# Kernel optimization log

Hardware: AMD Instinct MI355X
Metric: run time of the kernel (lower is better)

The kernel has to match this reference:

```python
import jax, jax.numpy as jnp
import numpy as np

B, N, HID = 2, 512, 768
BIAF = 256
CLS = 14
CH = 32
SIZE_DIM = 25
N_POS = 30
HSZ = 2 * (BIAF + 1) + SIZE_DIM


def setup_inputs() -> dict:
    key = jax.random.key(0)
    ks = jax.random.split(key, 16)
    s = 0.02
    return {
        "x": jax.random.normal(ks[0], (B, N, HID), jnp.float32),
        "y": jax.random.normal(ks[1], (B, N, HID), jnp.float32),
        "z": jax.random.normal(ks[2], (B, N, N, CH), jnp.float32),
        "mlp1_w": jax.random.normal(ks[3], (BIAF, HID), jnp.float32) * s,
        "mlp1_b": jnp.zeros((BIAF,), jnp.float32),
        "mlp2_w": jax.random.normal(ks[4], (BIAF, HID), jnp.float32) * s,
        "mlp2_b": jnp.zeros((BIAF,), jnp.float32),
        "head_w": jax.random.normal(ks[5], (BIAF, HID), jnp.float32) * s,
        "head_b": jnp.zeros((BIAF,), jnp.float32),
        "tail_w": jax.random.normal(ks[6], (BIAF, HID), jnp.float32) * s,
        "tail_b": jnp.zeros((BIAF,), jnp.float32),
        "biaf_W": jax.random.normal(ks[7], (CLS, BIAF + 1, BIAF + 1), jnp.float32) * s,
        "W": jax.random.normal(ks[8], (CLS, HSZ), jnp.float32) * s,
        "size_emb": jax.random.normal(ks[9], (N_POS, SIZE_DIM), jnp.float32) * s,
    }


def reference(x, y, z, mlp1_w, mlp1_b, mlp2_w, mlp2_b, head_w, head_b,
              tail_w, tail_b, biaf_W, W, size_emb):
    # MLP branches (dropout=0 at eval; torch GELU is exact erf)
    h = jax.nn.gelu(x @ mlp1_w.T + mlp1_b, approximate=False)   # (b,m,BIAF)
    t = jax.nn.gelu(y @ mlp2_w.T + mlp2_b, approximate=False)   # (b,n,BIAF)
    ones = jnp.ones(h.shape[:-1] + (1,), h.dtype)
    h1 = jnp.concatenate([h, ones], -1)                          # (b,m,BIAF+1)
    t1 = jnp.concatenate([t, ones], -1)                          # (b,n,BIAF+1)
    # Biaffine with bias_x=bias_y=True -> (b,cls,m,n)
    o1 = jnp.einsum('bmi,kij,bnj->bkmn', h1, biaf_W, t1)

    # head/tail MLPs with LeakyReLU(0.01), then append 1-column
    head = jax.nn.leaky_relu(x @ head_w.T + head_b, 0.01)
    tail = jax.nn.leaky_relu(x @ tail_w.T + tail_b, 0.01)
    head = jnp.concatenate([head, ones], -1)                     # (b,m,BIAF+1)
    tail = jnp.concatenate([tail, ones], -1)                     # (b,n,BIAF+1)

    # einsum('bmnh,kh->bkmn', cat([head_m, tail_n, size_mn]), W) decomposed so
    # the (b,m,n,HSZ) pairwise tensor is never materialized (same math).
    d = head.shape[-1]
    Wh, Wt, Ws = W[:, :d], W[:, d:2 * d], W[:, 2 * d:]
    n = x.shape[1]
    ar = jnp.arange(n)
    ids = jnp.clip(ar[None, :] - ar[:, None], -N_POS // 2, N_POS // 2 - 1) + N_POS // 2
    se = size_emb[ids]                                           # (m,n,SIZE_DIM)
    o3 = (jnp.einsum('bmh,kh->bkm', head, Wh)[:, :, :, None]
          + jnp.einsum('bnh,kh->bkn', tail, Wt)[:, :, None, :]
          + jnp.einsum('mnh,kh->kmn', se, Ws)[None])
    return o1 + o3
```

## Files before the change

### kernel.cpp

```cpp
#include <hip/hip_runtime.h>
#include <hip/hip_bf16.h>
#include <math.h>

#define BDIM 2
#define NDIM 512
#define HID 768
#define BIAF 256
#define CLS 14
#define DD 257
#define NPOS 30
#define SDIM 25
#define HSZ 539
#define PK 288
#define PJ 384
#define LDW 40

typedef unsigned short ushort_t;
typedef __attribute__((ext_vector_type(8))) short short8;
typedef __attribute__((ext_vector_type(4))) float floatx4;

#define MFMA16(a, b, c) __builtin_amdgcn_mfma_f32_16x16x32_bf16((a), (b), (c), 0, 0, 0)

__device__ inline float bf2f(ushort_t u) {
    union { unsigned int i; float f; } c; c.i = ((unsigned)u) << 16; return c.f;
}
__device__ inline ushort_t f2bf(float f) {
    __hip_bfloat16 h = __float2bfloat16(f);
    return *(ushort_t*)&h;
}

__device__ inline void split8(const float* v, short8& hi, short8& lo) {
    #pragma unroll
    for (int j = 0; j < 8; ++j) {
        ushort_t h = f2bf(v[j]);
        float hf = bf2f(h);
        ((short*)&hi)[j] = (short)h;
        ((short*)&lo)[j] = (short)f2bf(v[j] - hf);
    }
}

__device__ inline void stage_tile(const ushort_t* __restrict__ g, size_t gstride,
                                  ushort_t* __restrict__ lds, int tid) {
    int r0 = tid >> 2, c4 = tid & 3;
    #pragma unroll
    for (int i = 0; i < 2; ++i) {
        int row = i * 64 + r0;
        uint4 v = *(const uint4*)(g + (size_t)row * gstride + c4 * 8);
        *(uint4*)(lds + row * LDW + c4 * 8) = v;
    }
}

__global__ __launch_bounds__(256) void repack_t(
    const float* __restrict__ biafW, ushort_t* __restrict__ packW)
{
    __shared__ float tile[32][33];
    const int i0 = blockIdx.x * 32;
    const int j0 = blockIdx.y * 32;
    const int k  = blockIdx.z;
    const int r8 = threadIdx.x >> 5;
    const int c  = threadIdx.x & 31;
    #pragma unroll
    for (int rr = 0; rr < 4; ++rr) {
        int r = rr * 8 + r8;
        int gi = i0 + r, gj = j0 + c;
        tile[r][c] = (gi < DD && gj < DD) ? biafW[((size_t)k * DD + gi) * DD + gj] : 0.f;
    }
    __syncthreads();
    #pragma unroll
    for (int rr = 0; rr < 4; ++rr) {
        int jr = rr * 8 + r8;
        packW[((size_t)k * PJ + (j0 + jr)) * PK + i0 + c] = f2bf(tile[c][jr]);
    }
}

__global__ __launch_bounds__(256) void wsplit(
    const float* __restrict__ m1w, const float* __restrict__ m2w,
    const float* __restrict__ hw,  const float* __restrict__ tw,
    ushort_t* __restrict__ whi, ushort_t* __restrict__ wlo)
{
    int idx = blockIdx.x * 256 + threadIdx.x;
    int mat = idx / (BIAF * HID);
    int rem = idx % (BIAF * HID);
    const float* src = (mat == 0) ? m1w : (mat == 1) ? m2w : (mat == 2) ? hw : tw;
    float v = src[rem];
    ushort_t h = f2bf(v);
    whi[idx] = h;
    wlo[idx] = f2bf(v - bf2f(h));
}

__global__ void fill_pads(ushort_t* __restrict__ h1hi, ushort_t* __restrict__ h1lo,
                          ushort_t* __restrict__ t1hi, ushort_t* __restrict__ t1lo) {
    int idx = blockIdx.x * 256 + threadIdx.x;
    int plane = idx >> 15;
    int tok = (idx >> 5) & 1023;
    int c   = 256 + (idx & 31);
    ushort_t* dst = (plane == 0) ? h1hi : (plane == 1) ? h1lo : (plane == 2) ? t1hi : t1lo;
    ushort_t val = (c == 256 && (plane == 0 || plane == 2)) ? (ushort_t)0x3F80 : (ushort_t)0;
    dst[(size_t)tok * PK + c] = val;
}

__global__ __launch_bounds__(256) void proj_mfma(
    const float* __restrict__ x, const float* __restrict__ y,
    const ushort_t* __restrict__ whi, const ushort_t* __restrict__ wlo,
    const float* __restrict__ m1b, const float* __restrict__ m2b,
    const float* __restrict__ hb,  const float* __restrict__ tb,
    ushort_t* __restrict__ h1hi, ushort_t* __restrict__ h1lo,
    ushort_t* __restrict__ t1hi, ushort_t* __restrict__ t1lo,
    float* __restrict__ headf, float* __restrict__ tailf)
{
    const int bx = blockIdx.x;
    const int proj = bx >> 6;
    const int mt = (bx >> 2) & 15;
    const int ft = bx & 3;
    const int wave = threadIdx.x >> 6, L = threadIdx.x & 63;
    const int quad = L >> 4, l16 = L & 15;
    const int m0w = mt * 64 + wave * 16;
    const int f0 = ft * 64;

    const float* src  = (proj == 1) ? y : x;
    const float* bias = (proj == 0) ? m1b : (proj == 1) ? m2b : (proj == 2) ? hb : tb;

    const float* arow = src + (size_t)(m0w + l16) * HID + quad * 8;
    const size_t wbase = (size_t)proj * BIAF * HID;

    floatx4 acc[4];
    #pragma unroll
    for (int nf = 0; nf < 4; ++nf)
        #pragma unroll
        for (int r = 0; r < 4; ++r) acc[nf][r] = 0.f;

    for (int k0 = 0; k0 < HID; k0 += 32) {
        float av[8];
        *(float4*)&av[0] = *(const float4*)(arow + k0);
        *(float4*)&av[4] = *(const float4*)(arow + k0 + 4);
        short8 ahi, alo;
        split8(av, ahi, alo);
        #pragma unroll
        for (int nf = 0; nf < 4; ++nf) {
            size_t boff = wbase + (size_t)(f0 + nf * 16 + l16) * HID + quad * 8 + k0;
            short8 bhi = *(const short8*)(whi + boff);
            short8 blo = *(const short8*)(wlo + boff);
            acc[nf] = MFMA16(ahi, bhi, acc[nf]);
            acc[nf] = MFMA16(alo, bhi, acc[nf]);
            acc[nf] = MFMA16(ahi, blo, acc[nf]);
        }
    }

    #pragma unroll
    for (int nf = 0; nf < 4; ++nf) {
        int feat = f0 + nf * 16 + l16;
        float bv = bias[feat];
        #pragma unroll
        for (int r = 0; r < 4; ++r) {
            int tok = m0w + quad * 4 + r;
            float v = acc[nf][r] + bv;
            if (proj == 0) {
                float g = 0.5f * v * (1.0f + erff(v * 0.70710678118654752f));
                ushort_t h = f2bf(g);
                h1hi[(size_t)tok * PK + feat] = h;
                h1lo[(size_t)tok * PK + feat] = f2bf(g - bf2f(h));
            } else if (proj == 1) {
                float g = 0.5f * v * (1.0f + erff(v * 0.70710678118654752f));
                ushort_t h = f2bf(g);
                t1hi[(size_t)tok * PK + feat] = h;
                t1lo[(size_t)tok * PK + feat] = f2bf(g - bf2f(h));
            } else if (proj == 2) {
                headf[(size_t)tok * 256 + feat] = (v >= 0.f) ? v : 0.01f * v;
            } else {
                tailf[(size_t)tok * 256 + feat] = (v >= 0.f) ? v : 0.01f * v;
            }
        }
    }
}

__global__ __launch_bounds__(256) void hk_tk_kernel(
    const float* __restrict__ headf, const float* __restrict__ tailf,
    const float* __restrict__ W,
    float* __restrict__ hk, float* __restrict__ tk)
{
    int p = blockIdx.x * 256 + threadIdx.x;
    int which = p >> 14;
    int idx = p & 16383;
    int tok = idx >> 4;
    int k = idx & 15;
    if (k >= CLS) return;
    const float* row = (which ? tailf : headf) + (size_t)tok * 256;
    const float* wr = W + (size_t)k * HSZ + (which ? DD : 0);
    float acc = 0.f;
    for (int f4 = 0; f4 < 64; ++f4) {
        float4 rv = *(const float4*)(row + f4 * 4);
        acc += rv.x * wr[f4*4] + rv.y * wr[f4*4+1] + rv.z * wr[f4*4+2] + rv.w * wr[f4*4+3];
    }
    acc += wr[256];
    float* dst = which ? tk : hk;
    dst[(size_t)(tok >> 9) * CLS * NDIM + (size_t)k * NDIM + (tok & 511)] = acc;
}

__global__ void sk_kernel(const float* __restrict__ semb, const float* __restrict__ W,
                          float* __restrict__ sk)
{
    int idx = blockIdx.x * 256 + threadIdx.x;
    if (idx < CLS * NPOS) {
        int k = idx / NPOS, d = idx % NPOS;
        float acc = 0.f;
        for (int h = 0; h < SDIM; ++h)
            acc += semb[d*SDIM + h] * W[k*HSZ + 2*DD + h];
        sk[idx] = acc;
    }
}

__global__ __launch_bounds__(256) void mb_tile(
    const ushort_t* __restrict__ h1hi, const ushort_t* __restrict__ h1lo,
    const ushort_t* __restrict__ packW,
    ushort_t* __restrict__ Ab)
{
    __shared__ ushort_t lds[3 * 128 * LDW];
    ushort_t* Ahi = lds;
    ushort_t* Alo = lds + 128 * LDW;
    ushort_t* Bt  = lds + 2 * 128 * LDW;

    const int jt = blockIdx.x, mt = blockIdx.y, bk = blockIdx.z;
    const int b = bk / CLS, k = bk % CLS;
    const int tid = threadIdx.x;
    const int wave = tid >> 6, L = tid & 63;
    const int quad = L >> 4, l16 = L & 15;
    const int m0 = mt * 128;
    const int j0 = jt * 128;
    const int wm = (wave >> 1) * 64;
    const int wn = (wave & 1) * 64;

    const ushort_t* gA_hi = h1hi + (size_t)(b * NDIM + m0) * PK;
    const ushort_t* gA_lo = h1lo + (size_t)(b * NDIM + m0) * PK;
    const ushort_t* gB    = packW + ((size_t)k * PJ + j0) * PK;

    floatx4 acc[4][4];
    #pragma unroll
    for (int mi = 0; mi < 4; ++mi)
        #pragma unroll
        for (int ni = 0; ni < 4; ++ni)
            #pragma unroll
            for (int r = 0; r < 4; ++r) acc[mi][ni][r] = 0.f;

    for (int k0 = 0; k0 < PK; k0 += 32) {
        stage_tile(gA_hi + k0, PK, Ahi, tid);
        stage_tile(gA_lo + k0, PK, Alo, tid);
        stage_tile(gB + k0, PK, Bt, tid);
        __syncthreads();
        short8 ahi[4], alo[4], bb[4];
        #pragma unroll
        for (int i = 0; i < 4; ++i) {
            ahi[i] = *(const short8*)(Ahi + (wm + i * 16 + l16) * LDW + quad * 8);
            alo[i] = *(const short8*)(Alo + (wm + i * 16 + l16) * LDW + quad * 8);
            bb[i]  = *(const short8*)(Bt  + (wn + i * 16 + l16) * LDW + quad * 8);
        }
        #pragma unroll
        for (int mi = 0; mi < 4; ++mi)
            #pragma unroll
            for (int ni = 0; ni < 4; ++ni) {
                acc[mi][ni] = MFMA16(ahi[mi], bb[ni], acc[mi][ni]);
                acc[mi][ni] = MFMA16(alo[mi], bb[ni], acc[mi][ni]);
            }
        __syncthreads();
    }

    ushort_t* Aout = Ab + (size_t)bk * NDIM * PK;
    #pragma unroll
    for (int mi = 0; mi < 4; ++mi) {
        #pragma unroll
        for (int r = 0; r < 4; ++r) {
            int row = m0 + wm + mi * 16 + quad * 4 + r;
            #pragma unroll
            for (int ni = 0; ni < 4; ++ni) {
                int col = j0 + wn + ni * 16 + l16;
                if (col < PK) Aout[(size_t)row * PK + col] = f2bf(acc[mi][ni][r]);
            }
        }
    }
}

__global__ __launch_bounds__(256) void mo_tile(
    const ushort_t* __restrict__ Ab,
    const ushort_t* __restrict__ t1hi, const ushort_t* __restrict__ t1lo,
    const float* __restrict__ hk, const float* __restrict__ tk,
    const float* __restrict__ sk,
    float* __restrict__ out)
{
    __shared__ ushort_t lds[3 * 128 * LDW];
    __shared__ float skr[NPOS];
    ushort_t* At  = lds;
    ushort_t* Bhi = lds + 128 * LDW;
    ushort_t* Blo = lds + 2 * 128 * LDW;

    const int nt = blockIdx.x, mt = blockIdx.y, bk = blockIdx.z;
    const int b = bk / CLS, k = bk % CLS;
    const int tid = threadIdx.x;
    if (tid < NPOS) skr[tid] = sk[k * NPOS + tid];
    const int wave = tid >> 6, L = tid & 63;
    const int quad = L >> 4, l16 = L & 15;
    const int m0 = mt * 128;
    const int n0 = nt * 128;
    const int wm = (wave >> 1) * 64;
    const int wn = (wave & 1) * 64;

    const ushort_t* gA  = Ab + ((size_t)bk * NDIM + m0) * PK;
    const ushort_t* gBh = t1hi + (size_t)(b * NDIM + n0) * PK;
    const ushort_t* gBl = t1lo + (size_t)(b * NDIM + n0) * PK;

    floatx4 acc[4][4];
    #pragma unroll
    for (int mi = 0; mi < 4; ++mi)
        #pragma unroll
        for (int ni = 0; ni < 4; ++ni)
            #pragma unroll
            for (int r = 0; r < 4; ++r) acc[mi][ni][r] = 0.f;

    for (int k0 = 0; k0 < PK; k0 += 32) {
        stage_tile(gA + k0, PK, At, tid);
        stage_tile(gBh + k0, PK, Bhi, tid);
        stage_tile(gBl + k0, PK, Blo, tid);
        __syncthreads();
        short8 a[4], bh[4], bl[4];
        #pragma unroll
        for (int i = 0; i < 4; ++i) {
            a[i]  = *(const short8*)(At  + (wm + i * 16 + l16) * LDW + quad * 8);
            bh[i] = *(const short8*)(Bhi + (wn + i * 16 + l16) * LDW + quad * 8);
            bl[i] = *(const short8*)(Blo + (wn + i * 16 + l16) * LDW + quad * 8);
        }
        #pragma unroll
        for (int mi = 0; mi < 4; ++mi)
            #pragma unroll
            for (int ni = 0; ni < 4; ++ni) {
                acc[mi][ni] = MFMA16(a[mi], bh[ni], acc[mi][ni]);
                acc[mi][ni] = MFMA16(a[mi], bl[ni], acc[mi][ni]);
            }
        __syncthreads();
    }

    const size_t obase = (size_t)bk * NDIM;
    #pragma unroll
    for (int mi = 0; mi < 4; ++mi) {
        #pragma unroll
        for (int r = 0; r < 4; ++r) {
            int row = m0 + wm + mi * 16 + quad * 4 + r;
            float hv = hk[obase + row];
            #pragma unroll
            for (int ni = 0; ni < 4; ++ni) {
                int col = n0 + wn + ni * 16 + l16;
                int d = col - row; d = d < -15 ? -15 : (d > 14 ? 14 : d); d += 15;
                out[(obase + row) * NDIM + col] = acc[mi][ni][r] + hv + tk[obase + col] + skr[d];
            }
        }
    }
}

extern "C" void kernel_launch(void* const* d_in, const int* in_sizes, int n_in,
                              void* d_out, int out_size, void* d_ws, size_t ws_size,
                              hipStream_t stream) {
    const float* x    = (const float*)d_in[0];
    const float* y    = (const float*)d_in[1];
    const float* m1w  = (const float*)d_in[3];
    const float* m1b  = (const float*)d_in[4];
    const float* m2w  = (const float*)d_in[5];
    const float* m2b  = (const float*)d_in[6];
    const float* hw   = (const float*)d_in[7];
    const float* hb   = (const float*)d_in[8];
    const float* tw   = (const float*)d_in[9];
    const float* tb   = (const float*)d_in[10];
    const float* biafW= (const float*)d_in[11];
    const float* W    = (const float*)d_in[12];
    const float* semb = (const float*)d_in[13];

    char* p = (char*)d_ws;
    float* hk   = (float*)p;                    p += 57344;
    float* tk   = (float*)p;                    p += 57344;
    float* skp  = (float*)p;                    p += 2048;
    float* headf= (float*)p;                    p += 1048576;
    float* tailf= (float*)p;                    p += 1048576;
    ushort_t* h1hi = (ushort_t*)p;              p += 589824;
    ushort_t* h1lo = (ushort_t*)p;              p += 589824;
    ushort_t* t1hi = (ushort_t*)p;              p += 589824;
    ushort_t* t1lo = (ushort_t*)p;              p += 589824;
    ushort_t* packW= (ushort_t*)p;              p += 3096576;
    ushort_t* whi  = (ushort_t*)p;              p += 1572864;
    ushort_t* wlo  = (ushort_t*)p;              p += 1572864;
    ushort_t* Abuf = (ushort_t*)p;              p += 8257536;

    repack_t<<<dim3(9, 12, CLS), 256, 0, stream>>>(biafW, packW);
    wsplit<<<3072, 256, 0, stream>>>(m1w, m2w, hw, tw, whi, wlo);
    fill_pads<<<512, 256, 0, stream>>>(h1hi, h1lo, t1hi, t1lo);
    proj_mfma<<<256, 256, 0, stream>>>(x, y, whi, wlo, m1b, m2b, hb, tb,
                                       h1hi, h1lo, t1hi, t1lo, headf, tailf);
    hk_tk_kernel<<<128, 256, 0, stream>>>(headf, tailf, W, hk, tk);
    sk_kernel<<<2, 256, 0, stream>>>(semb, W, skp);
    mb_tile<<<dim3(3, 4, BDIM*CLS), 256, 0, stream>>>(h1hi, h1lo, packW, Abuf);
    mo_tile<<<dim3(4, 4, BDIM*CLS), 256, 0, stream>>>(Abuf, t1hi, t1lo, hk, tk, skp,
                                                      (float*)d_out);
}
```

Measured before the change: 214.5 us.

## Use direct global-to-LDS loads, smaller GEMM tiles, and pre-split x/y inputs

The two biaffine GEMM kernels now stage tiles with global_load_lds (16-byte direct-to-LDS copies) into unpadded LDS buffers instead of register round-trips. Tile sizes shrink to 64x96 and 64x128, doubling the block count so more CUs are busy. A new xysplit kernel converts x/y to bf16 hi/lo once, and proj_mfma uses a 3D grid with 32-feature tiles, giving more blocks. The trade-offs are an extra kernel launch and pass over x/y, possible LDS bank conflicts from the unpadded 32-wide rows, and less reuse per tile.

```diff
diff --git a/kernel.cpp b/kernel.cpp
--- a/kernel.cpp
+++ b/kernel.cpp
@@ -1,6 +1,7 @@
 #include <hip/hip_runtime.h>
 #include <hip/hip_bf16.h>
 #include <math.h>
+#include <stdint.h>
 
 #define BDIM 2
 #define NDIM 512
@@ -13,7 +14,6 @@
 #define HSZ 539
 #define PK 288
 #define PJ 384
-#define LDW 40
 
 typedef unsigned short ushort_t;
 typedef __attribute__((ext_vector_type(8))) short short8;
@@ -29,25 +29,11 @@
     return *(ushort_t*)&h;
 }
 
-__device__ inline void split8(const float* v, short8& hi, short8& lo) {
-    #pragma unroll
-    for (int j = 0; j < 8; ++j) {
-        ushort_t h = f2bf(v[j]);
-        float hf = bf2f(h);
-        ((short*)&hi)[j] = (short)h;
-        ((short*)&lo)[j] = (short)f2bf(v[j] - hf);
-    }
-}
-
-__device__ inline void stage_tile(const ushort_t* __restrict__ g, size_t gstride,
-                                  ushort_t* __restrict__ lds, int tid) {
-    int r0 = tid >> 2, c4 = tid & 3;
-    #pragma unroll
-    for (int i = 0; i < 2; ++i) {
-        int row = i * 64 + r0;
-        uint4 v = *(const uint4*)(g + (size_t)row * gstride + c4 * 8);
-        *(uint4*)(lds + row * LDW + c4 * 8) = v;
-    }
+__device__ inline void glds16(const ushort_t* g, const ushort_t* l) {
+    __builtin_amdgcn_global_load_lds(
+        (const __attribute__((address_space(1))) unsigned int*)(unsigned long long)(uintptr_t)g,
+        (__attribute__((address_space(3))) unsigned int*)(unsigned int)(uintptr_t)l,
+        16, 0, 0);
 }
 
 __global__ __launch_bounds__(256) void repack_t(
@@ -86,6 +72,20 @@
     ushort_t h = f2bf(v);
     whi[idx] = h;
     wlo[idx] = f2bf(v - bf2f(h));
+}
+
+__global__ __launch_bounds__(256) void xysplit(
+    const float* __restrict__ x, const float* __restrict__ y,
+    ushort_t* __restrict__ xhi, ushort_t* __restrict__ xlo,
+    ushort_t* __restrict__ yhi, ushort_t* __restrict__ ylo)
+{
+    int idx = blockIdx.x * 256 + threadIdx.x;
+    int which = idx >= (BDIM*NDIM*HID);
+    int rem = which ? idx - BDIM*NDIM*HID : idx;
+    float v = (which ? y : x)[rem];
+    ushort_t h = f2bf(v);
+    (which ? yhi : xhi)[rem] = h;
+    (which ? ylo : xlo)[rem] = f2bf(v - bf2f(h));
 }
 
 __global__ void fill_pads(ushort_t* __restrict__ h1hi, ushort_t* __restrict__ h1lo,
@@ -100,7 +100,8 @@
 }
 
 __global__ __launch_bounds__(256) void proj_mfma(
-    const float* __restrict__ x, const float* __restrict__ y,
+    const ushort_t* __restrict__ xhi, const ushort_t* __restrict__ xlo,
+    const ushort_t* __restrict__ yhi, const ushort_t* __restrict__ ylo,
     const ushort_t* __restrict__ whi, const ushort_t* __restrict__ wlo,
     const float* __restrict__ m1b, const float* __restrict__ m2b,
     const float* __restrict__ hb,  const float* __restrict__ tb,
@@ -108,66 +109,59 @@
     ushort_t* __restrict__ t1hi, ushort_t* __restrict__ t1lo,
     float* __restrict__ headf, float* __restrict__ tailf)
 {
-    const int bx = blockIdx.x;
-    const int proj = bx >> 6;
-    const int mt = (bx >> 2) & 15;
-    const int ft = bx & 3;
+    const int ft = blockIdx.x;
+    const int mt = blockIdx.y;
+    const int proj = blockIdx.z;
     const int wave = threadIdx.x >> 6, L = threadIdx.x & 63;
     const int quad = L >> 4, l16 = L & 15;
-    const int m0w = mt * 64 + wave * 16;
-    const int f0 = ft * 64;
-
-    const float* src  = (proj == 1) ? y : x;
+    const int tok0 = mt * 64 + wave * 16;
+    const int f0 = ft * 32;
+
+    const ushort_t* ahi_p = (proj == 1) ? yhi : xhi;
+    const ushort_t* alo_p = (proj == 1) ? ylo : xlo;
     const float* bias = (proj == 0) ? m1b : (proj == 1) ? m2b : (proj == 2) ? hb : tb;
 
-    const float* arow = src + (size_t)(m0w + l16) * HID + quad * 8;
+    const size_t aoff = (size_t)(tok0 + l16) * HID + quad * 8;
     const size_t wbase = (size_t)proj * BIAF * HID;
-
-    floatx4 acc[4];
-    #pragma unroll
-    for (int nf = 0; nf < 4; ++nf)
-        #pragma unroll
-        for (int r = 0; r < 4; ++r) acc[nf][r] = 0.f;
-
+    const size_t b0 = wbase + (size_t)(f0 + l16) * HID + quad * 8;
+    const size_t b1 = wbase + (size_t)(f0 + 16 + l16) * HID + quad * 8;
+
+    floatx4 acc0 = {0.f, 0.f, 0.f, 0.f}, acc1 = {0.f, 0.f, 0.f, 0.f};
+    #pragma unroll 4
     for (int k0 = 0; k0 < HID; k0 += 32) {
-        float av[8];
-        *(float4*)&av[0] = *(const float4*)(arow + k0);
-        *(float4*)&av[4] = *(const float4*)(arow + k0 + 4);
-        short8 ahi, alo;
-        split8(av, ahi, alo);
-        #pragma unroll
-        for (int nf = 0; nf < 4; ++nf) {
-            size_t boff = wbase + (size_t)(f0 + nf * 16 + l16) * HID + quad * 8 + k0;
-            short8 bhi = *(const short8*)(whi + boff);
-            short8 blo = *(const short8*)(wlo + boff);
-            acc[nf] = MFMA16(ahi, bhi, acc[nf]);
-            acc[nf] = MFMA16(alo, bhi, acc[nf]);
-            acc[nf] = MFMA16(ahi, blo, acc[nf]);
-        }
-    }
-
-    #pragma unroll
-    for (int nf = 0; nf < 4; ++nf) {
+        short8 ah  = *(const short8*)(ahi_p + aoff + k0);
+        short8 al  = *(const short8*)(alo_p + aoff + k0);
+        short8 bh0 = *(const short8*)(whi + b0 + k0);
+        short8 bl0 = *(const short8*)(wlo + b0 + k0);
+        short8 bh1 = *(const short8*)(whi + b1 + k0);
+        short8 bl1 = *(const short8*)(wlo + b1 + k0);
+        acc0 = MFMA16(ah, bh0, acc0);
+        acc1 = MFMA16(ah, bh1, acc1);
+        acc0 = MFMA16(al, bh0, acc0);
+        acc1 = MFMA16(al, bh1, acc1);
+        acc0 = MFMA16(ah, bl0, acc0);
+        acc1 = MFMA16(ah, bl1, acc1);
+    }
+
+    #pragma unroll
+    for (int nf = 0; nf < 2; ++nf) {
+        floatx4 a = nf ? acc1 : acc0;
         int feat = f0 + nf * 16 + l16;
         float bv = bias[feat];
         #pragma unroll
         for (int r = 0; r < 4; ++r) {
-            int tok = m0w + quad * 4 + r;
-            float v = acc[nf][r] + bv;
-            if (proj == 0) {
+            int tok = tok0 + quad * 4 + r;
+            float v = a[r] + bv;
+            if (proj <= 1) {
                 float g = 0.5f * v * (1.0f + erff(v * 0.70710678118654752f));
                 ushort_t h = f2bf(g);
-                h1hi[(size_t)tok * PK + feat] = h;
-                h1lo[(size_t)tok * PK + feat] = f2bf(g - bf2f(h));
-            } else if (proj == 1) {
-                float g = 0.5f * v * (1.0f + erff(v * 0.70710678118654752f));
-                ushort_t h = f2bf(g);
-                t1hi[(size_t)tok * PK + feat] = h;
-                t1lo[(size_t)tok * PK + feat] = f2bf(g - bf2f(h));
-            } else if (proj == 2) {
-                headf[(size_t)tok * 256 + feat] = (v >= 0.f) ? v : 0.01f * v;
+                ushort_t lo = f2bf(g - bf2f(h));
+                if (proj == 0) { h1hi[(size_t)tok * PK + feat] = h; h1lo[(size_t)tok * PK + feat] = lo; }
+                else           { t1hi[(size_t)tok * PK + feat] = h; t1lo[(size_t)tok * PK + feat] = lo; }
             } else {
-                tailf[(size_t)tok * 256 + feat] = (v >= 0.f) ? v : 0.01f * v;
+                float lv = (v >= 0.f) ? v : 0.01f * v;
+                if (proj == 2) headf[(size_t)tok * 256 + feat] = lv;
+                else           tailf[(size_t)tok * 256 + feat] = lv;
             }
         }
     }
@@ -214,65 +208,68 @@
     const ushort_t* __restrict__ packW,
     ushort_t* __restrict__ Ab)
 {
-    __shared__ ushort_t lds[3 * 128 * LDW];
-    ushort_t* Ahi = lds;
-    ushort_t* Alo = lds + 128 * LDW;
-    ushort_t* Bt  = lds + 2 * 128 * LDW;
-
+    __shared__ ushort_t Ah[64 * 32];
+    __shared__ ushort_t Al[64 * 32];
+    __shared__ ushort_t Bt[96 * 32];
     const int jt = blockIdx.x, mt = blockIdx.y, bk = blockIdx.z;
     const int b = bk / CLS, k = bk % CLS;
     const int tid = threadIdx.x;
     const int wave = tid >> 6, L = tid & 63;
     const int quad = L >> 4, l16 = L & 15;
-    const int m0 = mt * 128;
-    const int j0 = jt * 128;
-    const int wm = (wave >> 1) * 64;
-    const int wn = (wave & 1) * 64;
-
-    const ushort_t* gA_hi = h1hi + (size_t)(b * NDIM + m0) * PK;
-    const ushort_t* gA_lo = h1lo + (size_t)(b * NDIM + m0) * PK;
-    const ushort_t* gB    = packW + ((size_t)k * PJ + j0) * PK;
-
-    floatx4 acc[4][4];
-    #pragma unroll
-    for (int mi = 0; mi < 4; ++mi)
-        #pragma unroll
-        for (int ni = 0; ni < 4; ++ni)
+    const int lrow = L >> 2, lq = L & 3;
+    const int m0 = mt * 64, j0 = jt * 96;
+    const int wm = (wave >> 1) * 32, wj = (wave & 1) * 48;
+
+    const ushort_t* gAh = h1hi + (size_t)(b * NDIM + m0) * PK;
+    const ushort_t* gAl = h1lo + (size_t)(b * NDIM + m0) * PK;
+    const ushort_t* gB  = packW + ((size_t)k * PJ + j0) * PK;
+
+    floatx4 acc[2][3];
+    #pragma unroll
+    for (int mi = 0; mi < 2; ++mi)
+        #pragma unroll
+        for (int ni = 0; ni < 3; ++ni)
             #pragma unroll
             for (int r = 0; r < 4; ++r) acc[mi][ni][r] = 0.f;
 
     for (int k0 = 0; k0 < PK; k0 += 32) {
-        stage_tile(gA_hi + k0, PK, Ahi, tid);
-        stage_tile(gA_lo + k0, PK, Alo, tid);
-        stage_tile(gB + k0, PK, Bt, tid);
+        for (int s = wave; s < 14; s += 4) {
+            const ushort_t* g; const ushort_t* l;
+            if (s < 4)      { l = Ah + s * 512;       g = gAh + (size_t)(s * 16 + lrow) * PK + k0 + lq * 8; }
+            else if (s < 8) { l = Al + (s - 4) * 512; g = gAl + (size_t)((s - 4) * 16 + lrow) * PK + k0 + lq * 8; }
+            else            { l = Bt + (s - 8) * 512; g = gB  + (size_t)((s - 8) * 16 + lrow) * PK + k0 + lq * 8; }
+            glds16(g, l);
+        }
         __syncthreads();
-        short8 ahi[4], alo[4], bb[4];
-        #pragma unroll
-        for (int i = 0; i < 4; ++i) {
-            ahi[i] = *(const short8*)(Ahi + (wm + i * 16 + l16) * LDW + quad * 8);
-            alo[i] = *(const short8*)(Alo + (wm + i * 16 + l16) * LDW + quad * 8);
-            bb[i]  = *(const short8*)(Bt  + (wn + i * 16 + l16) * LDW + quad * 8);
-        }
-        #pragma unroll
-        for (int mi = 0; mi < 4; ++mi)
-            #pragma unroll
-            for (int ni = 0; ni < 4; ++ni) {
-                acc[mi][ni] = MFMA16(ahi[mi], bb[ni], acc[mi][ni]);
-                acc[mi][ni] = MFMA16(alo[mi], bb[ni], acc[mi][ni]);
+        short8 ah[2], al[2], bb[3];
+        #pragma unroll
+        for (int mi = 0; mi < 2; ++mi) {
+            ah[mi] = *(const short8*)(Ah + (wm + mi * 16 + l16) * 32 + quad * 8);
+            al[mi] = *(const short8*)(Al + (wm + mi * 16 + l16) * 32 + quad * 8);
+        }
+        #pragma unroll
+        for (int ni = 0; ni < 3; ++ni)
+            bb[ni] = *(const short8*)(Bt + (wj + ni * 16 + l16) * 32 + quad * 8);
+        #pragma unroll
+        for (int mi = 0; mi < 2; ++mi)
+            #pragma unroll
+            for (int ni = 0; ni < 3; ++ni) {
+                acc[mi][ni] = MFMA16(ah[mi], bb[ni], acc[mi][ni]);
+                acc[mi][ni] = MFMA16(al[mi], bb[ni], acc[mi][ni]);
             }
         __syncthreads();
     }
 
     ushort_t* Aout = Ab + (size_t)bk * NDIM * PK;
     #pragma unroll
-    for (int mi = 0; mi < 4; ++mi) {
+    for (int mi = 0; mi < 2; ++mi) {
         #pragma unroll
         for (int r = 0; r < 4; ++r) {
             int row = m0 + wm + mi * 16 + quad * 4 + r;
             #pragma unroll
-            for (int ni = 0; ni < 4; ++ni) {
-                int col = j0 + wn + ni * 16 + l16;
-                if (col < PK) Aout[(size_t)row * PK + col] = f2bf(acc[mi][ni][r]);
+            for (int ni = 0; ni < 3; ++ni) {
+                int col = j0 + wj + ni * 16 + l16;
+                Aout[(size_t)row * PK + col] = f2bf(acc[mi][ni][r]);
             }
         }
     }
@@ -285,49 +282,52 @@
     const float* __restrict__ sk,
     float* __restrict__ out)
 {
-    __shared__ ushort_t lds[3 * 128 * LDW];
+    __shared__ ushort_t At[64 * 32];
+    __shared__ ushort_t Bh[128 * 32];
+    __shared__ ushort_t Bl[128 * 32];
     __shared__ float skr[NPOS];
-    ushort_t* At  = lds;
-    ushort_t* Bhi = lds + 128 * LDW;
-    ushort_t* Blo = lds + 2 * 128 * LDW;
-
     const int nt = blockIdx.x, mt = blockIdx.y, bk = blockIdx.z;
     const int b = bk / CLS, k = bk % CLS;
     const int tid = threadIdx.x;
     if (tid < NPOS) skr[tid] = sk[k * NPOS + tid];
     const int wave = tid >> 6, L = tid & 63;
     const int quad = L >> 4, l16 = L & 15;
-    const int m0 = mt * 128;
-    const int n0 = nt * 128;
-    const int wm = (wave >> 1) * 64;
-    const int wn = (wave & 1) * 64;
+    const int lrow = L >> 2, lq = L & 3;
+    const int m0 = mt * 64, n0 = nt * 128;
+    const int wm = (wave >> 1) * 32, wn = (wave & 1) * 64;
 
     const ushort_t* gA  = Ab + ((size_t)bk * NDIM + m0) * PK;
     const ushort_t* gBh = t1hi + (size_t)(b * NDIM + n0) * PK;
     const ushort_t* gBl = t1lo + (size_t)(b * NDIM + n0) * PK;
 
-    floatx4 acc[4][4];
-    #pragma unroll
-    for (int mi = 0; mi < 4; ++mi)
+    floatx4 acc[2][4];
+    #pragma unroll
+    for (int mi = 0; mi < 2; ++mi)
         #pragma unroll
         for (int ni = 0; ni < 4; ++ni)
             #pragma unroll
             for (int r = 0; r < 4; ++r) acc[mi][ni][r] = 0.f;
 
     for (int k0 = 0; k0 < PK; k0 += 32) {
-        stage_tile(gA + k0, PK, At, tid);
-        stage_tile(gBh + k0, PK, Bhi, tid);
-        stage_tile(gBl + k0, PK, Blo, tid);
+        for (int s = wave; s < 20; s += 4) {
+            const ushort_t* g; const ushort_t* l;
+            if (s < 4)       { l = At + s * 512;        g = gA  + (size_t)(s * 16 + lrow) * PK + k0 + lq * 8; }
+            else if (s < 12) { l = Bh + (s - 4) * 512;  g = gBh + (size_t)((s - 4) * 16 + lrow) * PK + k0 + lq * 8; }
+            else             { l = Bl + (s - 12) * 512; g = gBl + (size_t)((s - 12) * 16 + lrow) * PK + k0 + lq * 8; }
+            glds16(g, l);
+        }
         __syncthreads();
-        short8 a[4], bh[4], bl[4];
-        #pragma unroll
-        for (int i = 0; i < 4; ++i) {
-            a[i]  = *(const short8*)(At  + (wm + i * 16 + l16) * LDW + quad * 8);
-            bh[i] = *(const short8*)(Bhi + (wn + i * 16 + l16) * LDW + quad * 8);
-            bl[i] = *(const short8*)(Blo + (wn + i * 16 + l16) * LDW + quad * 8);
-        }
-        #pragma unroll
-        for (int mi = 0; mi < 4; ++mi)
+        short8 a[2], bh[4], bl[4];
+        #pragma unroll
+        for (int mi = 0; mi < 2; ++mi)
+            a[mi] = *(const short8*)(At + (wm + mi * 16 + l16) * 32 + quad * 8);
+        #pragma unroll
+        for (int ni = 0; ni < 4; ++ni) {
+            bh[ni] = *(const short8*)(Bh + (wn + ni * 16 + l16) * 32 + quad * 8);
+            bl[ni] = *(const short8*)(Bl + (wn + ni * 16 + l16) * 32 + quad * 8);
+        }
+        #pragma unroll
+        for (int mi = 0; mi < 2; ++mi)
             #pragma unroll
             for (int ni = 0; ni < 4; ++ni) {
                 acc[mi][ni] = MFMA16(a[mi], bh[ni], acc[mi][ni]);
@@ -338,7 +338,7 @@
 
     const size_t obase = (size_t)bk * NDIM;
     #pragma unroll
-    for (int mi = 0; mi < 4; ++mi) {
+    for (int mi = 0; mi < 2; ++mi) {
         #pragma unroll
         for (int r = 0; r < 4; ++r) {
             int row = m0 + wm + mi * 16 + quad * 4 + r;
@@ -384,15 +384,21 @@
     ushort_t* whi  = (ushort_t*)p;              p += 1572864;
     ushort_t* wlo  = (ushort_t*)p;              p += 1572864;
     ushort_t* Abuf = (ushort_t*)p;              p += 8257536;
+    ushort_t* xhi  = (ushort_t*)p;              p += 1572864;
+    ushort_t* xlo  = (ushort_t*)p;              p += 1572864;
+    ushort_t* yhi  = (ushort_t*)p;              p += 1572864;
+    ushort_t* ylo  = (ushort_t*)p;              p += 1572864;
 
     repack_t<<<dim3(9, 12, CLS), 256, 0, stream>>>(biafW, packW);
     wsplit<<<3072, 256, 0, stream>>>(m1w, m2w, hw, tw, whi, wlo);
+    xysplit<<<6144, 256, 0, stream>>>(x, y, xhi, xlo, yhi, ylo);
     fill_pads<<<512, 256, 0, stream>>>(h1hi, h1lo, t1hi, t1lo);
-    proj_mfma<<<256, 256, 0, stream>>>(x, y, whi, wlo, m1b, m2b, hb, tb,
-                                       h1hi, h1lo, t1hi, t1lo, headf, tailf);
+    proj_mfma<<<dim3(8, 16, 4), 256, 0, stream>>>(xhi, xlo, yhi, ylo, whi, wlo,
+                                                  m1b, m2b, hb, tb,
+                                                  h1hi, h1lo, t1hi, t1lo, headf, tailf);
     hk_tk_kernel<<<128, 256, 0, stream>>>(headf, tailf, W, hk, tk);
     sk_kernel<<<2, 256, 0, stream>>>(semb, W, skp);
-    mb_tile<<<dim3(3, 4, BDIM*CLS), 256, 0, stream>>>(h1hi, h1lo, packW, Abuf);
-    mo_tile<<<dim3(4, 4, BDIM*CLS), 256, 0, stream>>>(Abuf, t1hi, t1lo, hk, tk, skp,
+    mb_tile<<<dim3(3, 8, BDIM*CLS), 256, 0, stream>>>(h1hi, h1lo, packW, Abuf);
+    mo_tile<<<dim3(4, 8, BDIM*CLS), 256, 0, stream>>>(Abuf, t1hi, t1lo, hk, tk, skp,
                                                       (float*)d_out);
 }
```

Measured after the change: 209.8 us. -2.2%, faster.
